# Kernel optimization log

Measured on AMD Instinct MI355X. Metric: run time of the kernel, lower is better.

## Reference

```python
import jax, jax.numpy as jnp
import numpy as np

HEAD_SIZE = 32


def setup_inputs() -> dict:
    key = jax.random.key(0)
    ks = jax.random.split(key, 9)
    B, N, M = 2, 512, 512
    Dq = Dk = Dv = 128
    De = 64
    H, O, OUT = 8, HEAD_SIZE, 128
    s = 0.05  # keep logits tame
    return {
        "query": jax.random.normal(ks[0], (B, N, Dq), jnp.float32),
        "key": jax.random.normal(ks[1], (B, M, Dk), jnp.float32),
        "value": jax.random.normal(ks[2], (B, M, Dv), jnp.float32),
        "edge": jax.random.normal(ks[3], (B, N, M, De), jnp.float32),
        "query_kernel": jax.random.normal(ks[4], (H, Dq, O), jnp.float32) * s,
        "key_kernel": jax.random.normal(ks[5], (H, Dk + De, O), jnp.float32) * s,
        "value_kernel": jax.random.normal(ks[6], (H, Dv, O), jnp.float32) * s,
        "projection_kernel": jax.random.normal(ks[7], (H, O, OUT), jnp.float32) * s,
        "projection_bias": jnp.zeros((OUT,), jnp.float32),
    }


def reference(query, key, value, edge, query_kernel, key_kernel,
              value_kernel, projection_kernel, projection_bias):
    # Edge-conditioned keys: concat broadcast key [B,1,M,Dk] with edge [B,N,M,De]
    B, N, _ = query.shape
    M = key.shape[-2]
    key_rep = jnp.broadcast_to(key[..., None, :, :], (B, N, M, key.shape[-1]))
    key_cat = jnp.concatenate([key_rep, edge], axis=-1)           # [B,N,M,Dk+De]
    k = jnp.einsum('bnmi,hio->bnmho', key_cat, key_kernel)        # [B,N,M,H,O]
    q = jnp.einsum('bni,hio->bnho', query, query_kernel)
    q = q / jnp.sqrt(jnp.asarray(HEAD_SIZE, q.dtype))
    v = jnp.einsum('bmi,hio->bmho', value, value_kernel)
    logits = jnp.einsum('bnho,bnmho->bhnm', q, k)                 # [B,H,N,M]
    attn = jax.nn.softmax(logits, axis=-1)
    mh = jnp.einsum('bhnm,bmho->bnho', attn, v)                   # [B,N,H,O]
    out = jnp.einsum('bnhi,hio->bno', mh, projection_kernel)
    out = out + projection_bias
    return out
```

## Files before the change

kernel.cpp:

```cpp
#include <hip/hip_runtime.h>
#include <hip/hip_bf16.h>

#define B_   2
#define N_   512
#define M_   512
#define D_   128
#define DE_  64
#define H_   8
#define O_   32
#define OUT_ 128
#define DKE_ 192
#define MP_  516

typedef unsigned short u16;
typedef unsigned int   u32;
typedef short bf16x8 __attribute__((ext_vector_type(8)));
typedef float floatx4 __attribute__((ext_vector_type(4)));

__device__ __forceinline__ u32 pk2bf(float a, float b) {
    __hip_bfloat162 h = __float22bfloat162_rn(make_float2(a, b));
    return *reinterpret_cast<u32*>(&h);
}
__device__ __forceinline__ u16 f2bf(float a) {
    __hip_bfloat16 h = __float2bfloat16(a);
    return *reinterpret_cast<u16*>(&h);
}
__device__ __forceinline__ bf16x8 cvt8(const float4 a, const float4 b) {
    union { u32 u[4]; bf16x8 v; } r;
    r.u[0] = pk2bf(a.x, a.y); r.u[1] = pk2bf(a.z, a.w);
    r.u[2] = pk2bf(b.x, b.y); r.u[3] = pk2bf(b.z, b.w);
    return r.v;
}

__global__ __launch_bounds__(256) void k_proj(
    const float* __restrict__ query, const float* __restrict__ Wq,
    const float* __restrict__ Wk,
    const float* __restrict__ value, const float* __restrict__ Wv,
    const float* __restrict__ key,
    u16* __restrict__ qE, u16* __restrict__ vP, u16* __restrict__ keyF)
{
    const int t = threadIdx.x;
    __shared__ float Xs[8][D_];
    __shared__ float qh[8][H_ * O_];

    if (blockIdx.x < 128) {
        const int r0 = blockIdx.x * 8;
        reinterpret_cast<float4*>(&Xs[0][0])[t] =
            reinterpret_cast<const float4*>(query + (size_t)r0 * D_)[t];
        __syncthreads();
        {
            float acc[8] = {0,0,0,0,0,0,0,0};
            const float* wcol = Wq + (t >> 5) * (D_ * O_) + (t & 31);
            for (int k = 0; k < D_; k += 4) {
                const float w0 = wcol[(k+0) * O_];
                const float w1 = wcol[(k+1) * O_];
                const float w2 = wcol[(k+2) * O_];
                const float w3 = wcol[(k+3) * O_];
#pragma unroll
                for (int r = 0; r < 8; ++r) {
                    const float4 x = *reinterpret_cast<const float4*>(&Xs[r][k]);
                    acc[r] += x.x * w0 + x.y * w1 + x.z * w2 + x.w * w3;
                }
            }
#pragma unroll
            for (int r = 0; r < 8; ++r) qh[r][t] = acc[r] * 0.17677669529663687f;
        }
        __syncthreads();

        for (int s = 0; s < 6; ++s) {
            const int hj = t + 256 * s;
            const int h  = hj / DKE_;
            float w[O_];
#pragma unroll
            for (int i = 0; i < O_ / 4; ++i) {
                const float4 x = reinterpret_cast<const float4*>(Wk + (size_t)hj * O_)[i];
                w[4*i] = x.x; w[4*i+1] = x.y; w[4*i+2] = x.z; w[4*i+3] = x.w;
            }
#pragma unroll
            for (int r = 0; r < 8; ++r) {
                const float* qrow = &qh[r][h * O_];
                float a = 0.f;
#pragma unroll
                for (int i = 0; i < O_ / 4; ++i) {
                    const float4 qx = *reinterpret_cast<const float4*>(qrow + 4*i);
                    a += qx.x * w[4*i] + qx.y * w[4*i+1] + qx.z * w[4*i+2] + qx.w * w[4*i+3];
                }
                qE[(size_t)(r0 + r) * (H_ * DKE_) + hj] = f2bf(a);
            }
        }
    } else if (blockIdx.x < 256) {
        const int r0 = (blockIdx.x - 128) * 8;
        reinterpret_cast<float4*>(&Xs[0][0])[t] =
            reinterpret_cast<const float4*>(value + (size_t)r0 * D_)[t];
        __syncthreads();

        float acc[8] = {0,0,0,0,0,0,0,0};
        const float* wcol = Wv + (t >> 5) * (D_ * O_) + (t & 31);
        for (int k = 0; k < D_; k += 4) {
            const float w0 = wcol[(k+0) * O_];
            const float w1 = wcol[(k+1) * O_];
            const float w2 = wcol[(k+2) * O_];
            const float w3 = wcol[(k+3) * O_];
#pragma unroll
            for (int r = 0; r < 8; ++r) {
                const float4 x = *reinterpret_cast<const float4*>(&Xs[r][k]);
                acc[r] += x.x * w0 + x.y * w1 + x.z * w2 + x.w * w3;
            }
        }
        const int bb = r0 >> 9, m0 = r0 & 511;
        union { u32 u[4]; uint4 q; } pk;
        pk.u[0] = pk2bf(acc[0], acc[1]);
        pk.u[1] = pk2bf(acc[2], acc[3]);
        pk.u[2] = pk2bf(acc[4], acc[5]);
        pk.u[3] = pk2bf(acc[6], acc[7]);
        *reinterpret_cast<uint4*>(
            vP + ((((size_t)bb * 64) + (m0 >> 3)) * 256 + t) * 8) = pk.q;
    } else {
        const int kb = blockIdx.x - 256;
        const int bb = kb >> 5, tl = kb & 31;
        const int kk = t >> 6, l = t & 63;
        const int br = l & 15, q = l >> 4;
        const float* src = key + ((size_t)bb * M_ + tl * 16 + br) * D_ + kk * 32 + q * 8;
        const float4 f0 = *reinterpret_cast<const float4*>(src);
        const float4 f1 = *reinterpret_cast<const float4*>(src + 4);
        union { bf16x8 v; uint4 u; } r;
        r.v = cvt8(f0, f1);
        *reinterpret_cast<uint4*>(
            keyF + ((((size_t)bb * 32 + tl) * 4 + kk) * 64 + l) * 8) = r.u;
    }
}

__global__ __launch_bounds__(256, 6) void k_attn(
    const float* __restrict__ edge,
    const u16* __restrict__ qE, const u16* __restrict__ vP,
    const u16* __restrict__ keyF,
    const float* __restrict__ Wp, const float* __restrict__ bias,
    float* __restrict__ out)
{
    const int idx  = blockIdx.x;
    const int b    = idx >> 9;
    const int t    = threadIdx.x;
    const int lane = t & 63;
    const int wv   = t >> 6;

    __shared__ __attribute__((aligned(16))) float attn_s[H_][MP_];
    __shared__ __attribute__((aligned(16))) u16 elds[4][1024];
    __shared__ float mh_s[H_ * O_];
    __shared__ float part_s[2][OUT_];

    const int br = lane & 15;
    const int q  = lane >> 4;

    const int base16 = ((lane >> 1) & 15) * 16 + ((lane >> 5) << 1) + (lane & 1);

    const float4* tb = reinterpret_cast<const float4*>(edge + (size_t)idx * (M_ * DE_));
    float4 ef[4];
#pragma unroll
    for (int i = 0; i < 4; ++i)
        ef[i] = tb[wv * 256 + base16 + i * 4];

    bf16x8 afr[6];
    if (br < 8) {
        const u16* ab = qE + (size_t)idx * (H_ * DKE_) + br * DKE_;
#pragma unroll
        for (int kk = 0; kk < 6; ++kk)
            afr[kk] = *reinterpret_cast<const bf16x8*>(ab + kk * 32 + q * 8);
    } else {
#pragma unroll
        for (int kk = 0; kk < 6; ++kk) afr[kk] = bf16x8{0,0,0,0,0,0,0,0};
    }

    const u16* kfb = keyF + (size_t)b * (32 * 4 * 64 * 8);

    for (int it = 0; it < 8; ++it) {
        const int tl = it * 4 + wv;
#pragma unroll
        for (int i = 0; i < 4; ++i) {
            uint2 p;
            p.x = pk2bf(ef[i].x, ef[i].y); p.y = pk2bf(ef[i].z, ef[i].w);
            *reinterpret_cast<uint2*>(&elds[wv][i * 256 + lane * 4]) = p;
        }
        if (it < 7) {
#pragma unroll
            for (int i = 0; i < 4; ++i)
                ef[i] = tb[(tl + 4) * 256 + base16 + i * 4];
        }
        floatx4 acc = {0.f, 0.f, 0.f, 0.f};
        const u16* kf = kfb + (size_t)tl * 2048 + lane * 8;
#pragma unroll
        for (int kk = 0; kk < 4; ++kk) {
            const bf16x8 bfr = *reinterpret_cast<const bf16x8*>(kf + kk * 512);
            acc = __builtin_amdgcn_mfma_f32_16x16x32_bf16(afr[kk], bfr, acc, 0, 0, 0);
        }
#pragma unroll
        for (int kk = 0; kk < 2; ++kk) {
            const bf16x8 bfr = *reinterpret_cast<const bf16x8*>(&elds[wv][(kk * 64 + lane) * 8]);
            acc = __builtin_amdgcn_mfma_f32_16x16x32_bf16(afr[4 + kk], bfr, acc, 0, 0, 0);
        }
        if (q < 2) {
#pragma unroll
            for (int i = 0; i < 4; ++i)
                attn_s[q * 4 + i][tl * 16 + br] = acc[i];
        }
    }
    __syncthreads();

    {
        const int h = t >> 5, ml = t & 31;
        float mx = -3.4e38f;
#pragma unroll 2
        for (int j = 0; j < 16; ++j) mx = fmaxf(mx, attn_s[h][ml + 32 * j]);
#pragma unroll
        for (int mask = 16; mask >= 1; mask >>= 1) mx = fmaxf(mx, __shfl_xor(mx, mask, 64));
        float sum = 0.f;
#pragma unroll 2
        for (int j = 0; j < 16; ++j) {
            const int m = ml + 32 * j;
            const float p = __expf(attn_s[h][m] - mx);
            attn_s[h][m] = p;
            sum += p;
        }
#pragma unroll
        for (int mask = 16; mask >= 1; mask >>= 1) sum += __shfl_xor(sum, mask, 64);
        const float inv = 1.f / sum;
#pragma unroll 2
        for (int j = 0; j < 16; ++j) attn_s[h][ml + 32 * j] *= inv;
    }
    __syncthreads();

    {
        const int hh = t >> 5;
        const u16* vb = vP + (size_t)b * (64 * 256 * 8) + (size_t)t * 8;
        float a0 = 0.f, a1 = 0.f;
#pragma unroll 8
        for (int j = 0; j < 64; ++j) {
            const uint4 v4 = *reinterpret_cast<const uint4*>(vb + (size_t)j * 2048);
            const float4 w0 = *reinterpret_cast<const float4*>(&attn_s[hh][j * 8]);
            const float4 w1 = *reinterpret_cast<const float4*>(&attn_s[hh][j * 8 + 4]);
            const float v0 = __uint_as_float(v4.x << 16);
            const float v1 = __uint_as_float(v4.x & 0xffff0000u);
            const float v2 = __uint_as_float(v4.y << 16);
            const float v3 = __uint_as_float(v4.y & 0xffff0000u);
            const float v4f = __uint_as_float(v4.z << 16);
            const float v5 = __uint_as_float(v4.z & 0xffff0000u);
            const float v6 = __uint_as_float(v4.w << 16);
            const float v7 = __uint_as_float(v4.w & 0xffff0000u);
            a0 += w0.x * v0 + w0.y * v1 + w0.z * v2 + w0.w * v3;
            a1 += w1.x * v4f + w1.y * v5 + w1.z * v6 + w1.w * v7;
        }
        mh_s[t] = a0 + a1;
    }
    __syncthreads();

    {
        const int half = t >> 7;
        const int c = t & 127;
        float acc = 0.f;
        const int j0 = half * 128;
#pragma unroll 8
        for (int jj = 0; jj < 128; ++jj)
            acc += mh_s[j0 + jj] * Wp[(size_t)(j0 + jj) * OUT_ + c];
        part_s[half][c] = acc;
    }
    __syncthreads();
    if (t < OUT_)
        out[(size_t)idx * OUT_ + t] = part_s[0][t] + part_s[1][t] + bias[t];
}

extern "C" void kernel_launch(void* const* d_in, const int* in_sizes, int n_in,
                              void* d_out, int out_size, void* d_ws, size_t ws_size,
                              hipStream_t stream)
{
    const float* query = (const float*)d_in[0];
    const float* key   = (const float*)d_in[1];
    const float* value = (const float*)d_in[2];
    const float* edge  = (const float*)d_in[3];
    const float* Wq    = (const float*)d_in[4];
    const float* Wk    = (const float*)d_in[5];
    const float* Wv    = (const float*)d_in[6];
    const float* Wp    = (const float*)d_in[7];
    const float* bias  = (const float*)d_in[8];
    float* out = (float*)d_out;

    u16* qE_ws = (u16*)d_ws;
    u16* vP_ws = qE_ws + (size_t)B_ * N_ * H_ * DKE_;
    u16* kF_ws = vP_ws + (size_t)B_ * 64 * 256 * 8;

    k_proj<<<320,  256, 0, stream>>>(query, Wq, Wk, value, Wv, key, qE_ws, vP_ws, kF_ws);
    k_attn<<<1024, 256, 0, stream>>>(edge, qE_ws, vP_ws, kF_ws, Wp, bias, out);
}
```

Measured before the change: 249.9 us.

## Double attention block size to 512 threads, splitting each stage across eight waves

The attention kernel now runs 512 threads per row block. Eight waves each handle four key tiles instead of four waves handling eight. Softmax maps one wave per head, and the PV and projection reductions are split in halves and quarters with extra shared-memory partial sums. The aim is more memory-level parallelism on the dominant edge stream and shorter serial loops per block. The cost is a higher register constraint from launch bounds (512,8) and extra LDS per block, which may limit residency.

```diff
diff --git a/kernel.cpp b/kernel.cpp
--- a/kernel.cpp
+++ b/kernel.cpp
@@ -130,7 +130,7 @@
     }
 }
 
-__global__ __launch_bounds__(256, 6) void k_attn(
+__global__ __launch_bounds__(512, 8) void k_attn(
     const float* __restrict__ edge,
     const u16* __restrict__ qE, const u16* __restrict__ vP,
     const u16* __restrict__ keyF,
@@ -144,9 +144,9 @@
     const int wv   = t >> 6;
 
     __shared__ __attribute__((aligned(16))) float attn_s[H_][MP_];
-    __shared__ __attribute__((aligned(16))) u16 elds[4][1024];
-    __shared__ float mh_s[H_ * O_];
-    __shared__ float part_s[2][OUT_];
+    __shared__ __attribute__((aligned(16))) u16 elds[8][1024];
+    __shared__ float mh_s[2][256];
+    __shared__ float part_s[4][OUT_];
 
     const int br = lane & 15;
     const int q  = lane >> 4;
@@ -172,18 +172,18 @@
 
     const u16* kfb = keyF + (size_t)b * (32 * 4 * 64 * 8);
 
-    for (int it = 0; it < 8; ++it) {
-        const int tl = it * 4 + wv;
+    for (int it = 0; it < 4; ++it) {
+        const int tl = it * 8 + wv;
 #pragma unroll
         for (int i = 0; i < 4; ++i) {
             uint2 p;
             p.x = pk2bf(ef[i].x, ef[i].y); p.y = pk2bf(ef[i].z, ef[i].w);
             *reinterpret_cast<uint2*>(&elds[wv][i * 256 + lane * 4]) = p;
         }
-        if (it < 7) {
+        if (it < 3) {
 #pragma unroll
             for (int i = 0; i < 4; ++i)
-                ef[i] = tb[(tl + 4) * 256 + base16 + i * 4];
+                ef[i] = tb[(tl + 8) * 256 + base16 + i * 4];
         }
         floatx4 acc = {0.f, 0.f, 0.f, 0.f};
         const u16* kf = kfb + (size_t)tl * 2048 + lane * 8;
@@ -206,37 +206,40 @@
     __syncthreads();
 
     {
-        const int h = t >> 5, ml = t & 31;
+        const int h = wv, ml = lane;
         float mx = -3.4e38f;
-#pragma unroll 2
-        for (int j = 0; j < 16; ++j) mx = fmaxf(mx, attn_s[h][ml + 32 * j]);
-#pragma unroll
-        for (int mask = 16; mask >= 1; mask >>= 1) mx = fmaxf(mx, __shfl_xor(mx, mask, 64));
+#pragma unroll
+        for (int j = 0; j < 8; ++j) mx = fmaxf(mx, attn_s[h][ml + 64 * j]);
+#pragma unroll
+        for (int mask = 32; mask >= 1; mask >>= 1) mx = fmaxf(mx, __shfl_xor(mx, mask, 64));
         float sum = 0.f;
-#pragma unroll 2
-        for (int j = 0; j < 16; ++j) {
-            const int m = ml + 32 * j;
+#pragma unroll
+        for (int j = 0; j < 8; ++j) {
+            const int m = ml + 64 * j;
             const float p = __expf(attn_s[h][m] - mx);
             attn_s[h][m] = p;
             sum += p;
         }
 #pragma unroll
-        for (int mask = 16; mask >= 1; mask >>= 1) sum += __shfl_xor(sum, mask, 64);
+        for (int mask = 32; mask >= 1; mask >>= 1) sum += __shfl_xor(sum, mask, 64);
         const float inv = 1.f / sum;
-#pragma unroll 2
-        for (int j = 0; j < 16; ++j) attn_s[h][ml + 32 * j] *= inv;
+#pragma unroll
+        for (int j = 0; j < 8; ++j) attn_s[h][ml + 64 * j] *= inv;
     }
     __syncthreads();
 
     {
-        const int hh = t >> 5;
-        const u16* vb = vP + (size_t)b * (64 * 256 * 8) + (size_t)t * 8;
+        const int tt = t & 255, half = t >> 8, hh = tt >> 5;
+        const u16* vb = vP + (size_t)b * (64 * 256 * 8)
+                      + ((size_t)(half * 32) * 256 + tt) * 8;
+        const int mbase = half * 256;
         float a0 = 0.f, a1 = 0.f;
 #pragma unroll 8
-        for (int j = 0; j < 64; ++j) {
+        for (int j = 0; j < 32; ++j) {
             const uint4 v4 = *reinterpret_cast<const uint4*>(vb + (size_t)j * 2048);
-            const float4 w0 = *reinterpret_cast<const float4*>(&attn_s[hh][j * 8]);
-            const float4 w1 = *reinterpret_cast<const float4*>(&attn_s[hh][j * 8 + 4]);
+            const int m0 = mbase + j * 8;
+            const float4 w0 = *reinterpret_cast<const float4*>(&attn_s[hh][m0]);
+            const float4 w1 = *reinterpret_cast<const float4*>(&attn_s[hh][m0 + 4]);
             const float v0 = __uint_as_float(v4.x << 16);
             const float v1 = __uint_as_float(v4.x & 0xffff0000u);
             const float v2 = __uint_as_float(v4.y << 16);
@@ -248,23 +251,25 @@
             a0 += w0.x * v0 + w0.y * v1 + w0.z * v2 + w0.w * v3;
             a1 += w1.x * v4f + w1.y * v5 + w1.z * v6 + w1.w * v7;
         }
-        mh_s[t] = a0 + a1;
+        mh_s[half][tt] = a0 + a1;
     }
     __syncthreads();
 
     {
-        const int half = t >> 7;
-        const int c = t & 127;
+        const int seg = t >> 7, c = t & 127;
+        const int j0 = seg * 64;
         float acc = 0.f;
-        const int j0 = half * 128;
 #pragma unroll 8
-        for (int jj = 0; jj < 128; ++jj)
-            acc += mh_s[j0 + jj] * Wp[(size_t)(j0 + jj) * OUT_ + c];
-        part_s[half][c] = acc;
+        for (int jj = 0; jj < 64; ++jj) {
+            const int j = j0 + jj;
+            acc += (mh_s[0][j] + mh_s[1][j]) * Wp[(size_t)j * OUT_ + c];
+        }
+        part_s[seg][c] = acc;
     }
     __syncthreads();
     if (t < OUT_)
-        out[(size_t)idx * OUT_ + t] = part_s[0][t] + part_s[1][t] + bias[t];
+        out[(size_t)idx * OUT_ + t] = part_s[0][t] + part_s[1][t]
+                                    + part_s[2][t] + part_s[3][t] + bias[t];
 }
 
 extern "C" void kernel_launch(void* const* d_in, const int* in_sizes, int n_in,
@@ -287,5 +292,5 @@
     u16* kF_ws = vP_ws + (size_t)B_ * 64 * 256 * 8;
 
     k_proj<<<320,  256, 0, stream>>>(query, Wq, Wk, value, Wv, key, qE_ws, vP_ws, kF_ws);
-    k_attn<<<1024, 256, 0, stream>>>(edge, qE_ws, vP_ws, kF_ws, Wp, bias, out);
-}
+    k_attn<<<1024, 512, 0, stream>>>(edge, qE_ws, vP_ws, kF_ws, Wp, bias, out);
+}
```

Measured after the change: 241.9 us. 3.2% less time.
